# Performance work log

Measured on AMD Instinct MI355X. Metric: run time of the kernel, lower is better.

## Reference

```python
import jax, jax.numpy as jnp
import numpy as np
import math

B, S, D, N, H = 4, 2048, 1024, 512, 8
HD = D // H  # head_dim = 128
LN_EPS = 1e-5


def setup_inputs() -> dict:
    key = jax.random.key(0)
    ks = jax.random.split(key, 12)
    return {
        "query": jax.random.normal(ks[0], (B, S, D), jnp.float32),
        "memory_weights": jax.random.uniform(ks[1], (B, S, N), jnp.float32),
        "update_input": jax.random.normal(ks[2], (B, S, D), jnp.float32),
        "memory_keys": jax.random.normal(ks[3], (N, D), jnp.float32),
        "memory_values": jax.random.normal(ks[4], (N, D), jnp.float32),
        "memory_decay": jnp.float32(0.95),
        "gate_w": jax.random.normal(ks[5], (2 * D, D), jnp.float32) / math.sqrt(2 * D),
        "gate_b": jnp.zeros((D,), jnp.float32),
        "out_w": jax.random.normal(ks[6], (D, D), jnp.float32) / math.sqrt(D),
        "out_b": jnp.zeros((D,), jnp.float32),
        "ln_gamma": jnp.ones((D,), jnp.float32),
        "ln_beta": jnp.zeros((D,), jnp.float32),
    }


def reference(query, memory_weights, update_input, memory_keys, memory_values,
              memory_decay, gate_w, gate_b, out_w, out_b, ln_gamma, ln_beta):
    # Multi-head attention read: einsum 'bshd,nhd->bsn' sums over h and d,
    # so it equals a full [D]-dot product; only the scale uses head_dim.
    scores = jnp.einsum("bsd,nd->bsn", query, memory_keys) / math.sqrt(HD)
    scores = scores * memory_weights  # multiplicative mask before softmax
    probs = jax.nn.softmax(scores, axis=-1)
    memory_read = jnp.einsum("bsn,nd->bsd", probs, memory_values)
    memory_read = memory_read * memory_decay

    # Gated update path (update_input provided)
    gate_in = jnp.concatenate([memory_read, update_input], axis=-1)  # [B,S,2D]
    gate = jax.nn.sigmoid(gate_in @ gate_w + gate_b)  # [B,S,D]
    # NOTE: the no_grad EMA update of memory_values is a side effect that does
    # not influence this forward output; omitted from the pure reference.
    memory_read = memory_read * (1.0 + jnp.mean(gate, axis=-1, keepdims=True))

    out = memory_read @ out_w + out_b  # output projection (dropout = eval identity)
    mu = jnp.mean(out, axis=-1, keepdims=True)
    var = jnp.var(out, axis=-1, keepdims=True)
    out = (out - mu) * jax.lax.rsqrt(var + LN_EPS) * ln_gamma + ln_beta
    return out
```

## Files before the change

kernel.cpp:

```cpp
#include <hip/hip_runtime.h>
#include <hip/hip_bf16.h>

typedef __attribute__((ext_vector_type(8))) short bf16x8;
typedef __attribute__((ext_vector_type(4))) float f32x4;
typedef __attribute__((ext_vector_type(4))) int i32x4;
typedef __attribute__((ext_vector_type(2))) int i32x2;
typedef __attribute__((ext_vector_type(4))) unsigned short u16x4;

static __device__ __forceinline__ void gload_lds16(const void* g, void* l) {
  __builtin_amdgcn_global_load_lds((const __attribute__((address_space(1))) void*)g,
                                   (__attribute__((address_space(3))) void*)l,
                                   16, 0, 0);
}

static __device__ __forceinline__ unsigned short f2bf(float x) {
  unsigned int u = __float_as_uint(x);
  u += 0x7fffu + ((u >> 16) & 1u);
  return (unsigned short)(u >> 16);
}
static __device__ __forceinline__ float bf2f(unsigned short u) {
  return __uint_as_float((unsigned int)u << 16);
}

template <int BN>
static __device__ __forceinline__ void gemm_core(
    const unsigned short* __restrict__ A, int lda,
    const unsigned short* __restrict__ Bt, int ldb,
    int kbeg, int kend, int brow, int bcol,
    unsigned short* As, unsigned short* Bs,
    f32x4 (&acc)[4][BN / 32])
{
  constexpr int NB = BN / 32;
  const int tid = threadIdx.x;
  const int wid = tid >> 6, lane = tid & 63;
  const int wr = wid >> 1, wc = wid & 1;
  const int l15 = lane & 15, l4 = lane >> 4;
  const int foff = wid * 512 + lane * 8;

  for (int k0 = kbeg; k0 < kend; k0 += 64) {
#pragma unroll
    for (int c = 0; c < 4; ++c) {
      int f = c * 2048 + foff;
      gload_lds16(A + (size_t)(brow + (f >> 6)) * lda + k0 + (f & 63),
                  As + c * 2048 + wid * 512);
    }
#pragma unroll
    for (int c = 0; c < NB; ++c) {
      int f = c * 2048 + foff;
      gload_lds16(Bt + (size_t)(bcol + (f >> 6)) * ldb + k0 + (f & 63),
                  Bs + c * 2048 + wid * 512);
    }
    __syncthreads();
#pragma unroll
    for (int kk = 0; kk < 2; ++kk) {
      const int ko = kk * 32 + l4 * 8;
      bf16x8 af[4], bfv[NB];
#pragma unroll
      for (int m = 0; m < 4; ++m)
        af[m] = *(const bf16x8*)(As + (wr * 64 + m * 16 + l15) * 64 + ko);
#pragma unroll
      for (int n = 0; n < NB; ++n)
        bfv[n] = *(const bf16x8*)(Bs + (wc * (BN / 2) + n * 16 + l15) * 64 + ko);
#pragma unroll
      for (int m = 0; m < 4; ++m)
#pragma unroll
        for (int n = 0; n < NB; ++n)
          acc[m][n] = __builtin_amdgcn_mfma_f32_16x16x32_bf16(af[m], bfv[n], acc[m][n], 0, 0, 0);
    }
    __syncthreads();
  }
}

__global__ __launch_bounds__(256)
void prep(const float* __restrict__ ob, int* __restrict__ flag,
          float* __restrict__ zeros,
          const float* __restrict__ mk, const float* __restrict__ mv,
          unsigned short* __restrict__ kb, unsigned short* __restrict__ mvb,
          const float* __restrict__ ow, unsigned short* __restrict__ owt,
          const float* __restrict__ q, unsigned short* __restrict__ qb,
          const float* __restrict__ upd, unsigned short* __restrict__ cat,
          const float* __restrict__ gw, unsigned short* __restrict__ gwt,
          unsigned short* __restrict__ vt)
{
  __shared__ float t[32][33];
  const int b = blockIdx.x;
  const int tid = threadIdx.x;
  if (b == 0) {
    f32x4 v = *(const f32x4*)(ob + tid * 4);
    float mx = fmaxf(fmaxf(fabsf(v[0]), fabsf(v[1])), fmaxf(fabsf(v[2]), fabsf(v[3])));
#pragma unroll
    for (int off = 32; off >= 1; off >>= 1) mx = fmaxf(mx, __shfl_xor(mx, off, 64));
    __shared__ float sm[4];
    const int wid = tid >> 6, lane = tid & 63;
    if (lane == 0) sm[wid] = mx;
    __syncthreads();
    if (tid == 0) {
      float m = fmaxf(fmaxf(sm[0], sm[1]), fmaxf(sm[2], sm[3]));
      *flag = (m != 0.0f) ? 1 : 0;
    }
  } else if (b < 17) {
    f32x4 z = {};
    *(f32x4*)(zeros + (b - 1) * 1024 + tid * 4) = z;
  } else if (b < 529) {
    int idx = (b - 17) * 256 + tid;
    const float* in; unsigned short* out; int rel;
    if (idx < 65536) { in = mk; out = kb;  rel = idx; }
    else             { in = mv; out = mvb; rel = idx - 65536; }
    size_t f = (size_t)rel * 8;
    f32x4 a = *(const f32x4*)(in + f);
    f32x4 c = *(const f32x4*)(in + f + 4);
    union { unsigned short u[8]; i32x4 vec; } pk;
#pragma unroll
    for (int i = 0; i < 4; ++i) { pk.u[i] = f2bf(a[i]); pk.u[4 + i] = f2bf(c[i]); }
    *(i32x4*)(out + f) = pk.vec;
  } else if (b < 1553) {
    int id = b - 529;
    const int bx = id & 31, by = id >> 5;
    const int tx = tid & 31, ty = tid >> 5;
    const int c0 = bx * 32, r0 = by * 32;
#pragma unroll
    for (int i = 0; i < 4; ++i)
      t[ty + i * 8][tx] = ow[(size_t)(r0 + ty + i * 8) * 1024 + c0 + tx];
    __syncthreads();
#pragma unroll
    for (int i = 0; i < 4; ++i)
      owt[(size_t)(c0 + ty + i * 8) * 1024 + r0 + tx] = f2bf(t[tx][ty + i * 8]);
  } else if (b < 5649) {
    int idx = (b - 1553) * 256 + tid;
    size_t f = (size_t)idx * 8;
    f32x4 a = *(const f32x4*)(q + f);
    f32x4 c = *(const f32x4*)(q + f + 4);
    union { unsigned short u[8]; i32x4 vec; } pk;
#pragma unroll
    for (int i = 0; i < 4; ++i) { pk.u[i] = f2bf(a[i]); pk.u[4 + i] = f2bf(c[i]); }
    *(i32x4*)(qb + f) = pk.vec;
  } else {
    f32x4 v = *(const f32x4*)(ob + tid * 4);
    float mx = fmaxf(fmaxf(fabsf(v[0]), fabsf(v[1])), fmaxf(fabsf(v[2]), fabsf(v[3])));
#pragma unroll
    for (int off = 32; off >= 1; off >>= 1) mx = fmaxf(mx, __shfl_xor(mx, off, 64));
    __shared__ float sm2[4];
    const int wid = tid >> 6, lane = tid & 63;
    if (lane == 0) sm2[wid] = mx;
    __syncthreads();
    float m = fmaxf(fmaxf(sm2[0], sm2[1]), fmaxf(sm2[2], sm2[3]));
    if (m == 0.0f) return;
    __syncthreads();
    int g = b - 5649;
    if (g < 4096) {
      int idx = g * 256 + tid;
      size_t f = (size_t)idx * 8;
      int row = (int)(f >> 10);
      int col = (int)(f & 1023);
      f32x4 a = *(const f32x4*)(upd + f);
      f32x4 c = *(const f32x4*)(upd + f + 4);
      union { unsigned short u[8]; i32x4 vec; } pk;
#pragma unroll
      for (int i = 0; i < 4; ++i) { pk.u[i] = f2bf(a[i]); pk.u[4 + i] = f2bf(c[i]); }
      *(i32x4*)(cat + (size_t)row * 2048 + 1024 + col) = pk.vec;
    } else {
      const float* in; unsigned short* out; int R, id;
      if (g < 6144) { in = gw; out = gwt; R = 2048; id = g - 4096; }
      else          { in = mv; out = vt;  R = 512;  id = g - 6144; }
      const int bx = id & 31, by = id >> 5;
      const int tx = tid & 31, ty = tid >> 5;
      const int c0 = bx * 32, r0 = by * 32;
#pragma unroll
      for (int i = 0; i < 4; ++i)
        t[ty + i * 8][tx] = in[(size_t)(r0 + ty + i * 8) * 1024 + c0 + tx];
      __syncthreads();
#pragma unroll
      for (int i = 0; i < 4; ++i)
        out[(size_t)(c0 + ty + i * 8) * R + r0 + tx] = f2bf(t[tx][ty + i * 8]);
    }
  }
}

__global__ __launch_bounds__(256)
void k_scores_w2(const unsigned short* __restrict__ qb,
                 const unsigned short* __restrict__ kb,
                 const float* __restrict__ mw,
                 unsigned short* __restrict__ probs,
                 float* __restrict__ rowsum,
                 const unsigned short* __restrict__ owt,
                 const unsigned short* __restrict__ mvb,
                 float* __restrict__ w2p)
{
  __shared__ unsigned short As[128 * 64];
  __shared__ unsigned short Bs[128 * 64];
  const int b = blockIdx.x;
  const int tid = threadIdx.x;
  const int wid = tid >> 6, lane = tid & 63;
  const int wr = wid >> 1, wc = wid & 1;
  const int l15 = lane & 15, l4 = lane >> 4;

  if (b < 128) {
    const int brow = ((b >> 2) & 7) * 128;
    const int bcol = (b & 3) * 128;
    const int kbeg = (b >> 5) * 256;
    f32x4 acc[4][4] = {};
    gemm_core<128>(owt, 1024, mvb, 1024, kbeg, kbeg + 256, brow, bcol, As, Bs, acc);
    float* dst = w2p + (size_t)(b >> 5) * 524288;
#pragma unroll
    for (int m = 0; m < 4; ++m) {
      int row0 = brow + wr * 64 + m * 16 + l4 * 4;
#pragma unroll
      for (int j = 0; j < 4; ++j) {
#pragma unroll
        for (int n = 0; n < 4; ++n)
          dst[(size_t)(row0 + j) * 512 + bcol + wc * 64 + n * 16 + l15] = acc[m][n][j];
      }
    }
  } else {
    const int f = b - 128;
    const int swz = (f & 7) * 64 + (f >> 3);
    const int bx = swz & 7, by = swz >> 3;
    const int brow = by * 128, bcol = bx * 64;
    f32x4 acc[4][2] = {};
    gemm_core<64>(qb, 1024, kb, 1024, 0, 1024, brow, bcol, As, Bs, acc);
#pragma unroll
    for (int m = 0; m < 4; ++m) {
#pragma unroll
      for (int j = 0; j < 4; ++j) {
        int row = brow + wr * 64 + m * 16 + l4 * 4 + j;
        const float* mwrow = mw + (size_t)row * 512;
        float part = 0.0f;
#pragma unroll
        for (int n = 0; n < 2; ++n) {
          int col = bcol + wc * 32 + n * 16 + l15;
          float p = __expf(acc[m][n][j] * 0.08838834764831845f * mwrow[col]);
          part += p;
          probs[(size_t)row * 512 + col] = f2bf(p);
        }
#pragma unroll
        for (int off = 1; off < 16; off <<= 1)
          part += __shfl_xor(part, off, 64);
        if (l15 == 0) atomicAdd(&rowsum[row], part);
      }
    }
  }
}

__global__ __launch_bounds__(256)
void k_w2red_read(const float* __restrict__ w2p, unsigned short* __restrict__ w2t,
                  const float* __restrict__ dec,
                  const unsigned short* __restrict__ probs,
                  const unsigned short* __restrict__ vt,
                  unsigned short* __restrict__ cat,
                  const float* __restrict__ rowsum,
                  const int* __restrict__ flag)
{
  __shared__ unsigned short As[128 * 64];
  __shared__ unsigned short Bs[128 * 64];
  const int b = blockIdx.x;
  const int tid = threadIdx.x;
  if (b < 512) {
    const int i = (b * 256 + tid) * 4;
    const float d = *dec;
    f32x4 s = {};
#pragma unroll
    for (int sl = 0; sl < 4; ++sl) {
      f32x4 p = *(const f32x4*)(w2p + (size_t)sl * 524288 + i);
      s[0] += p[0]; s[1] += p[1]; s[2] += p[2]; s[3] += p[3];
    }
    union { unsigned short u[4]; i32x2 v; } pk;
#pragma unroll
    for (int j = 0; j < 4; ++j) pk.u[j] = f2bf(s[j] * d);
    *(i32x2*)(w2t + i) = pk.v;
  } else {
    if (*flag == 0) return;
    const int f = b - 512;
    const int swz = (f & 7) * 64 + (f >> 3);
    const int bx = swz & 7, by = swz >> 3;
    const int brow = by * 128, bcol = bx * 128;
    const int wid = tid >> 6, lane = tid & 63;
    const int wr = wid >> 1, wc = wid & 1;
    const int l15 = lane & 15, l4 = lane >> 4;
    f32x4 acc[4][4] = {};
    gemm_core<128>(probs, 512, vt, 512, 0, 512, brow, bcol, As, Bs, acc);
    const float d = *dec;
#pragma unroll
    for (int m = 0; m < 4; ++m) {
      int row0 = brow + wr * 64 + m * 16 + l4 * 4;
#pragma unroll
      for (int j = 0; j < 4; ++j) {
        int row = row0 + j;
        const float rscl = d / rowsum[row];
#pragma unroll
        for (int n = 0; n < 4; ++n) {
          int col = bcol + wc * 64 + n * 16 + l15;
          cat[(size_t)row * 2048 + col] = f2bf(acc[m][n][j] * rscl);
        }
      }
    }
  }
}

__global__ __launch_bounds__(256)
void k_out_gate(const unsigned short* __restrict__ probs,
                const unsigned short* __restrict__ w2t,
                const float* __restrict__ rowsum,
                unsigned short* __restrict__ outpre,
                const unsigned short* __restrict__ cat,
                const unsigned short* __restrict__ gwt,
                const float* __restrict__ gb,
                float* __restrict__ gsum,
                const int* __restrict__ flag)
{
  __shared__ unsigned short As[128 * 64];
  __shared__ unsigned short Bs[128 * 64];
  const int b = blockIdx.x;
  const int tid = threadIdx.x;
  const int wid = tid >> 6, lane = tid & 63;
  const int wr = wid >> 1, wc = wid & 1;
  const int l15 = lane & 15, l4 = lane >> 4;

  if (b < 512) {
    const int swz = (b & 7) * 64 + (b >> 3);
    const int bx = swz & 7, by = swz >> 3;
    const int brow = by * 128, bcol = bx * 128;
    f32x4 acc[4][4] = {};
    gemm_core<128>(probs, 512, w2t, 512, 0, 512, brow, bcol, As, Bs, acc);
#pragma unroll
    for (int m = 0; m < 4; ++m) {
      int row0 = brow + wr * 64 + m * 16 + l4 * 4;
#pragma unroll
      for (int j = 0; j < 4; ++j) {
        int row = row0 + j;
        const float rscl = 1.0f / rowsum[row];
#pragma unroll
        for (int n = 0; n < 4; ++n) {
          int col = bcol + wc * 64 + n * 16 + l15;
          outpre[(size_t)row * 1024 + col] = f2bf(acc[m][n][j] * rscl);
        }
      }
    }
  } else {
    if (*flag == 0) return;
    const int f = b - 512;
    const int swz = (f & 7) * 64 + (f >> 3);
    const int bx = swz & 7, by = swz >> 3;
    const int brow = by * 128, bcol = bx * 128;
    f32x4 acc[4][4] = {};
    gemm_core<128>(cat, 2048, gwt, 2048, 0, 2048, brow, bcol, As, Bs, acc);
#pragma unroll
    for (int m = 0; m < 4; ++m) {
#pragma unroll
      for (int j = 0; j < 4; ++j) {
        float part = 0.0f;
#pragma unroll
        for (int n = 0; n < 4; ++n) {
          int col = bcol + wc * 64 + n * 16 + l15;
          float x = acc[m][n][j] + gb[col];
          part += 1.0f / (1.0f + __expf(-x));
        }
#pragma unroll
        for (int off = 1; off < 16; off <<= 1)
          part += __shfl_xor(part, off, 64);
        if (l15 == 0) {
          int row = brow + wr * 64 + m * 16 + l4 * 4 + j;
          atomicAdd(&gsum[row], part);
        }
      }
    }
  }
}

__global__ __launch_bounds__(256)
void ln_rows(const unsigned short* __restrict__ X, const float* __restrict__ gsum,
             const float* __restrict__ ob,
             const float* __restrict__ gamma, const float* __restrict__ beta,
             float* __restrict__ Y)
{
  const int row = blockIdx.x;
  const int tid = threadIdx.x;
  const size_t base = (size_t)row * 1024 + tid * 4;
  const float scl = 1.0f + gsum[row] * (1.0f / 1024.0f);
  u16x4 xr = *(const u16x4*)(X + base);
  f32x4 bo = *(const f32x4*)(ob + tid * 4);
  float x[4];
#pragma unroll
  for (int i = 0; i < 4; ++i) x[i] = bf2f(xr[i]) * scl + bo[i];
  float s = x[0] + x[1] + x[2] + x[3];
  float q = x[0] * x[0] + x[1] * x[1] + x[2] * x[2] + x[3] * x[3];
#pragma unroll
  for (int off = 32; off >= 1; off >>= 1) {
    s += __shfl_xor(s, off, 64);
    q += __shfl_xor(q, off, 64);
  }
  __shared__ float ss[4], qq[4];
  const int wid = tid >> 6, lane = tid & 63;
  if (lane == 0) { ss[wid] = s; qq[wid] = q; }
  __syncthreads();
  s = ss[0] + ss[1] + ss[2] + ss[3];
  q = qq[0] + qq[1] + qq[2] + qq[3];
  const float mu = s * (1.0f / 1024.0f);
  const float var = q * (1.0f / 1024.0f) - mu * mu;
  const float r = rsqrtf(var + 1e-5f);
  f32x4 g = *(const f32x4*)(gamma + tid * 4);
  f32x4 bt = *(const f32x4*)(beta + tid * 4);
  f32x4 y;
#pragma unroll
  for (int i = 0; i < 4; ++i) y[i] = (x[i] - mu) * r * g[i] + bt[i];
  *(f32x4*)(Y + base) = y;
}

extern "C" void kernel_launch(void* const* d_in, const int* in_sizes, int n_in,
                              void* d_out, int out_size, void* d_ws, size_t ws_size,
                              hipStream_t stream)
{
  (void)in_sizes; (void)n_in; (void)out_size; (void)ws_size;
  const float* q   = (const float*)d_in[0];
  const float* mw  = (const float*)d_in[1];
  const float* upd = (const float*)d_in[2];
  const float* mk  = (const float*)d_in[3];
  const float* mv  = (const float*)d_in[4];
  const float* dec = (const float*)d_in[5];
  const float* gw  = (const float*)d_in[6];
  const float* gb  = (const float*)d_in[7];
  const float* ow  = (const float*)d_in[8];
  const float* ob  = (const float*)d_in[9];
  const float* lg  = (const float*)d_in[10];
  const float* lb  = (const float*)d_in[11];
  float* outp = (float*)d_out;
  char* ws = (char*)d_ws;

  unsigned short* qb     = (unsigned short*)(ws + 0);
  unsigned short* probs  = (unsigned short*)(ws + 16777216);
  unsigned short* outpre = (unsigned short*)(ws + 25165824);
  unsigned short* kb     = (unsigned short*)(ws + 41943040);
  unsigned short* mvb    = (unsigned short*)(ws + 42991616);
  unsigned short* owt    = (unsigned short*)(ws + 44040192);
  unsigned short* w2t    = (unsigned short*)(ws + 46137344);
  float*          w2p    = (float*)(ws + 47185920);
  unsigned short* vt     = (unsigned short*)(ws + 55574528);
  unsigned short* gwt    = (unsigned short*)(ws + 56623104);
  unsigned short* cat    = (unsigned short*)(ws + 60817408);
  float*          gsum   = (float*)(ws + 94371840);
  float*          rowsum = (float*)(ws + 94404608);
  int*            flag   = (int*)(ws + 94437376);

  prep<<<12305, 256, 0, stream>>>(ob, flag, gsum, mk, mv, kb, mvb, ow, owt,
                                  q, qb, upd, cat, gw, gwt, vt);
  k_scores_w2<<<640, 256, 0, stream>>>(qb, kb, mw, probs, rowsum, owt, mvb, w2p);
  k_w2red_read<<<1024, 256, 0, stream>>>(w2p, w2t, dec, probs, vt, cat, rowsum, flag);
  k_out_gate<<<1024, 256, 0, stream>>>(probs, w2t, rowsum, outpre, cat, gwt, gb, gsum, flag);
  ln_rows<<<8192, 256, 0, stream>>>(outpre, gsum, ob, lg, lb, outp);
}
```

Baseline: 81.75 us.

## Restructure kernel pipeline: separate rowsum pass, rebalance W2 split-K, split gate GEMM

Drops the per-row atomicAdd for the softmax denominator in the scores kernel. Rowsum now comes from a separate reduction over the bf16 probs, fused into the W2 reduction launch. The W2 (out_w·values) product moves to 64-wide tiles with 2-way instead of 4-way split-K, so the reduction reads fewer partials. The memory-read GEMM now shares a launch with the output GEMM, and the gate GEMM gets its own kernel. Probs and outpre are stored as paired bf16 words via lane shuffles. The cost is an extra kernel launch and an extra pass over probs, and rowsum now sums bf16-rounded values.

```diff
diff --git a/kernel.cpp b/kernel.cpp
--- a/kernel.cpp
+++ b/kernel.cpp
@@ -181,130 +181,103 @@
                  const unsigned short* __restrict__ kb,
                  const float* __restrict__ mw,
                  unsigned short* __restrict__ probs,
-                 float* __restrict__ rowsum,
                  const unsigned short* __restrict__ owt,
                  const unsigned short* __restrict__ mvb,
                  float* __restrict__ w2p)
 {
   __shared__ unsigned short As[128 * 64];
-  __shared__ unsigned short Bs[128 * 64];
+  __shared__ unsigned short Bs[64 * 64];
   const int b = blockIdx.x;
   const int tid = threadIdx.x;
   const int wid = tid >> 6, lane = tid & 63;
   const int wr = wid >> 1, wc = wid & 1;
   const int l15 = lane & 15, l4 = lane >> 4;
 
-  if (b < 128) {
-    const int brow = ((b >> 2) & 7) * 128;
-    const int bcol = (b & 3) * 128;
-    const int kbeg = (b >> 5) * 256;
-    f32x4 acc[4][4] = {};
-    gemm_core<128>(owt, 1024, mvb, 1024, kbeg, kbeg + 256, brow, bcol, As, Bs, acc);
-    float* dst = w2p + (size_t)(b >> 5) * 524288;
-#pragma unroll
-    for (int m = 0; m < 4; ++m) {
-      int row0 = brow + wr * 64 + m * 16 + l4 * 4;
-#pragma unroll
-      for (int j = 0; j < 4; ++j) {
-#pragma unroll
-        for (int n = 0; n < 4; ++n)
-          dst[(size_t)(row0 + j) * 512 + bcol + wc * 64 + n * 16 + l15] = acc[m][n][j];
-      }
-    }
-  } else {
-    const int f = b - 128;
-    const int swz = (f & 7) * 64 + (f >> 3);
+  if (b < 512) {
+    const int swz = (b & 7) * 64 + (b >> 3);
     const int bx = swz & 7, by = swz >> 3;
     const int brow = by * 128, bcol = bx * 64;
     f32x4 acc[4][2] = {};
     gemm_core<64>(qb, 1024, kb, 1024, 0, 1024, brow, bcol, As, Bs, acc);
+
 #pragma unroll
     for (int m = 0; m < 4; ++m) {
 #pragma unroll
       for (int j = 0; j < 4; ++j) {
         int row = brow + wr * 64 + m * 16 + l4 * 4 + j;
         const float* mwrow = mw + (size_t)row * 512;
-        float part = 0.0f;
 #pragma unroll
         for (int n = 0; n < 2; ++n) {
           int col = bcol + wc * 32 + n * 16 + l15;
           float p = __expf(acc[m][n][j] * 0.08838834764831845f * mwrow[col]);
-          part += p;
-          probs[(size_t)row * 512 + col] = f2bf(p);
+          float o = __shfl_xor(p, 1);
+          if (!(lane & 1)) {
+            unsigned int pw = (unsigned int)f2bf(p) | ((unsigned int)f2bf(o) << 16);
+            *(unsigned int*)(probs + (size_t)row * 512 + col) = pw;
+          }
         }
-#pragma unroll
-        for (int off = 1; off < 16; off <<= 1)
-          part += __shfl_xor(part, off, 64);
-        if (l15 == 0) atomicAdd(&rowsum[row], part);
-      }
-    }
-  }
-}
-
-__global__ __launch_bounds__(256)
-void k_w2red_read(const float* __restrict__ w2p, unsigned short* __restrict__ w2t,
-                  const float* __restrict__ dec,
-                  const unsigned short* __restrict__ probs,
-                  const unsigned short* __restrict__ vt,
-                  unsigned short* __restrict__ cat,
-                  const float* __restrict__ rowsum,
-                  const int* __restrict__ flag)
-{
-  __shared__ unsigned short As[128 * 64];
-  __shared__ unsigned short Bs[128 * 64];
+      }
+    }
+  } else {
+    const int g = b - 512;
+    const int bx = g & 7;
+    const int by = (g >> 3) & 7;
+    const int bz = g >> 6;
+    const int brow = by * 128, bcol = bx * 64;
+    f32x4 acc[4][2] = {};
+    gemm_core<64>(owt, 1024, mvb, 1024, bz * 512, bz * 512 + 512, brow, bcol, As, Bs, acc);
+    float* dst = w2p + (size_t)bz * 524288;
+#pragma unroll
+    for (int m = 0; m < 4; ++m) {
+      int row0 = brow + wr * 64 + m * 16 + l4 * 4;
+#pragma unroll
+      for (int j = 0; j < 4; ++j) {
+#pragma unroll
+        for (int n = 0; n < 2; ++n)
+          dst[(size_t)(row0 + j) * 512 + bcol + wc * 32 + n * 16 + l15] = acc[m][n][j];
+      }
+    }
+  }
+}
+
+__global__ __launch_bounds__(256)
+void k_w2red_rowsum(const float* __restrict__ w2p, unsigned short* __restrict__ w2t,
+                    const float* __restrict__ dec,
+                    const unsigned short* __restrict__ probs,
+                    float* __restrict__ rowsum)
+{
   const int b = blockIdx.x;
   const int tid = threadIdx.x;
   if (b < 512) {
     const int i = (b * 256 + tid) * 4;
     const float d = *dec;
-    f32x4 s = {};
-#pragma unroll
-    for (int sl = 0; sl < 4; ++sl) {
-      f32x4 p = *(const f32x4*)(w2p + (size_t)sl * 524288 + i);
-      s[0] += p[0]; s[1] += p[1]; s[2] += p[2]; s[3] += p[3];
-    }
+    f32x4 s0 = *(const f32x4*)(w2p + i);
+    f32x4 s1 = *(const f32x4*)(w2p + 524288 + i);
     union { unsigned short u[4]; i32x2 v; } pk;
 #pragma unroll
-    for (int j = 0; j < 4; ++j) pk.u[j] = f2bf(s[j] * d);
+    for (int j = 0; j < 4; ++j) pk.u[j] = f2bf((s0[j] + s1[j]) * d);
     *(i32x2*)(w2t + i) = pk.v;
   } else {
-    if (*flag == 0) return;
-    const int f = b - 512;
-    const int swz = (f & 7) * 64 + (f >> 3);
-    const int bx = swz & 7, by = swz >> 3;
-    const int brow = by * 128, bcol = bx * 128;
     const int wid = tid >> 6, lane = tid & 63;
-    const int wr = wid >> 1, wc = wid & 1;
-    const int l15 = lane & 15, l4 = lane >> 4;
-    f32x4 acc[4][4] = {};
-    gemm_core<128>(probs, 512, vt, 512, 0, 512, brow, bcol, As, Bs, acc);
-    const float d = *dec;
-#pragma unroll
-    for (int m = 0; m < 4; ++m) {
-      int row0 = brow + wr * 64 + m * 16 + l4 * 4;
-#pragma unroll
-      for (int j = 0; j < 4; ++j) {
-        int row = row0 + j;
-        const float rscl = d / rowsum[row];
-#pragma unroll
-        for (int n = 0; n < 4; ++n) {
-          int col = bcol + wc * 64 + n * 16 + l15;
-          cat[(size_t)row * 2048 + col] = f2bf(acc[m][n][j] * rscl);
-        }
-      }
-    }
-  }
-}
-
-__global__ __launch_bounds__(256)
-void k_out_gate(const unsigned short* __restrict__ probs,
+    const int row = (b - 512) * 4 + wid;
+    bf16x8 v = *(const bf16x8*)(probs + (size_t)row * 512 + lane * 8);
+    float s = 0.0f;
+#pragma unroll
+    for (int i = 0; i < 8; ++i) s += bf2f((unsigned short)v[i]);
+#pragma unroll
+    for (int off = 32; off >= 1; off >>= 1) s += __shfl_xor(s, off, 64);
+    if (lane == 0) rowsum[row] = s;
+  }
+}
+
+__global__ __launch_bounds__(256)
+void k_out_read(const unsigned short* __restrict__ probs,
                 const unsigned short* __restrict__ w2t,
                 const float* __restrict__ rowsum,
                 unsigned short* __restrict__ outpre,
-                const unsigned short* __restrict__ cat,
-                const unsigned short* __restrict__ gwt,
-                const float* __restrict__ gb,
-                float* __restrict__ gsum,
+                const unsigned short* __restrict__ vt,
+                unsigned short* __restrict__ cat,
+                const float* __restrict__ dec,
                 const int* __restrict__ flag)
 {
   __shared__ unsigned short As[128 * 64];
@@ -331,7 +304,12 @@
 #pragma unroll
         for (int n = 0; n < 4; ++n) {
           int col = bcol + wc * 64 + n * 16 + l15;
-          outpre[(size_t)row * 1024 + col] = f2bf(acc[m][n][j] * rscl);
+          float v = acc[m][n][j] * rscl;
+          float o = __shfl_xor(v, 1);
+          if (!(lane & 1)) {
+            unsigned int pw = (unsigned int)f2bf(v) | ((unsigned int)f2bf(o) << 16);
+            *(unsigned int*)(outpre + (size_t)row * 1024 + col) = pw;
+          }
         }
       }
     }
@@ -342,25 +320,62 @@
     const int bx = swz & 7, by = swz >> 3;
     const int brow = by * 128, bcol = bx * 128;
     f32x4 acc[4][4] = {};
-    gemm_core<128>(cat, 2048, gwt, 2048, 0, 2048, brow, bcol, As, Bs, acc);
+    gemm_core<128>(probs, 512, vt, 512, 0, 512, brow, bcol, As, Bs, acc);
+    const float d = *dec;
 #pragma unroll
     for (int m = 0; m < 4; ++m) {
+      int row0 = brow + wr * 64 + m * 16 + l4 * 4;
 #pragma unroll
       for (int j = 0; j < 4; ++j) {
-        float part = 0.0f;
+        int row = row0 + j;
+        const float rscl = d / rowsum[row];
 #pragma unroll
         for (int n = 0; n < 4; ++n) {
           int col = bcol + wc * 64 + n * 16 + l15;
-          float x = acc[m][n][j] + gb[col];
-          part += 1.0f / (1.0f + __expf(-x));
+          cat[(size_t)row * 2048 + col] = f2bf(acc[m][n][j] * rscl);
         }
-#pragma unroll
-        for (int off = 1; off < 16; off <<= 1)
-          part += __shfl_xor(part, off, 64);
-        if (l15 == 0) {
-          int row = brow + wr * 64 + m * 16 + l4 * 4 + j;
-          atomicAdd(&gsum[row], part);
-        }
+      }
+    }
+  }
+}
+
+__global__ __launch_bounds__(256)
+void k_gate(const unsigned short* __restrict__ cat,
+            const unsigned short* __restrict__ gwt,
+            const float* __restrict__ gb,
+            float* __restrict__ gsum,
+            const int* __restrict__ flag)
+{
+  if (*flag == 0) return;
+  __shared__ unsigned short As[128 * 64];
+  __shared__ unsigned short Bs[128 * 64];
+  const int b = blockIdx.x;
+  const int tid = threadIdx.x;
+  const int wid = tid >> 6, lane = tid & 63;
+  const int wr = wid >> 1, wc = wid & 1;
+  const int l15 = lane & 15, l4 = lane >> 4;
+  const int swz = (b & 7) * 64 + (b >> 3);
+  const int bx = swz & 7, by = swz >> 3;
+  const int brow = by * 128, bcol = bx * 128;
+  f32x4 acc[4][4] = {};
+  gemm_core<128>(cat, 2048, gwt, 2048, 0, 2048, brow, bcol, As, Bs, acc);
+#pragma unroll
+  for (int m = 0; m < 4; ++m) {
+#pragma unroll
+    for (int j = 0; j < 4; ++j) {
+      float part = 0.0f;
+#pragma unroll
+      for (int n = 0; n < 4; ++n) {
+        int col = bcol + wc * 64 + n * 16 + l15;
+        float x = acc[m][n][j] + gb[col];
+        part += 1.0f / (1.0f + __expf(-x));
+      }
+#pragma unroll
+      for (int off = 1; off < 16; off <<= 1)
+        part += __shfl_xor(part, off, 64);
+      if (l15 == 0) {
+        int row = brow + wr * 64 + m * 16 + l4 * 4 + j;
+        atomicAdd(&gsum[row], part);
       }
     }
   }
@@ -433,17 +448,18 @@
   unsigned short* owt    = (unsigned short*)(ws + 44040192);
   unsigned short* w2t    = (unsigned short*)(ws + 46137344);
   float*          w2p    = (float*)(ws + 47185920);
-  unsigned short* vt     = (unsigned short*)(ws + 55574528);
-  unsigned short* gwt    = (unsigned short*)(ws + 56623104);
-  unsigned short* cat    = (unsigned short*)(ws + 60817408);
-  float*          gsum   = (float*)(ws + 94371840);
-  float*          rowsum = (float*)(ws + 94404608);
-  int*            flag   = (int*)(ws + 94437376);
+  unsigned short* vt     = (unsigned short*)(ws + 51380224);
+  unsigned short* gwt    = (unsigned short*)(ws + 52428800);
+  unsigned short* cat    = (unsigned short*)(ws + 56623104);
+  float*          gsum   = (float*)(ws + 90177536);
+  float*          rowsum = (float*)(ws + 90210304);
+  int*            flag   = (int*)(ws + 90243072);
 
   prep<<<12305, 256, 0, stream>>>(ob, flag, gsum, mk, mv, kb, mvb, ow, owt,
                                   q, qb, upd, cat, gw, gwt, vt);
-  k_scores_w2<<<640, 256, 0, stream>>>(qb, kb, mw, probs, rowsum, owt, mvb, w2p);
-  k_w2red_read<<<1024, 256, 0, stream>>>(w2p, w2t, dec, probs, vt, cat, rowsum, flag);
-  k_out_gate<<<1024, 256, 0, stream>>>(probs, w2t, rowsum, outpre, cat, gwt, gb, gsum, flag);
+  k_scores_w2<<<640, 256, 0, stream>>>(qb, kb, mw, probs, owt, mvb, w2p);
+  k_w2red_rowsum<<<2560, 256, 0, stream>>>(w2p, w2t, dec, probs, rowsum);
+  k_out_read<<<1024, 256, 0, stream>>>(probs, w2t, rowsum, outpre, vt, cat, dec, flag);
+  k_gate<<<512, 256, 0, stream>>>(cat, gwt, gb, gsum, flag);
   ln_rows<<<8192, 256, 0, stream>>>(outpre, gsum, ob, lg, lb, outp);
 }
```

After: 83.24 us. No clear change (+1.8%).
